# Kernel tuning notes

Measured on AMD Instinct MI355X. Metric: run time of the kernel, lower is better.

The kernel has to match this reference:

```python
import jax, jax.numpy as jnp
import numpy as np

DYNAMIC_RANGE = 16  # from init_kwargs
MAX_VAL = 2 ** (DYNAMIC_RANGE - 1) - 1   # 32767
MIN_VAL = -(2 ** (DYNAMIC_RANGE - 1))    # -32768


def setup_inputs() -> dict:
    key = jax.random.key(0)
    k_img, k_w = jax.random.split(key)
    Z, Y, X = 128, 512, 512
    P = 15                      # prediction_bands
    image = jax.random.normal(k_img, (Z, Y, X), dtype=jnp.float32) * 100.0
    # weights buffer is [num_bands, 4 + prediction_bands]; original inits to zeros
    # (degenerate output), so we use small random weights in [-1, 1].
    weights = jax.random.normal(k_w, (Z, 4 + P), dtype=jnp.float32) * 0.05
    return {"image": image, "weights": weights}


def reference(image, weights):
    # image: [Z, Y, X], weights: [Z, 4 + P]
    Z, Y, X = image.shape
    P = weights.shape[1] - 4

    # Note: sample_representatives[z] = predictions[z] + residuals[z] = image[z],
    # so all neighbor extraction operates on the raw image. Weight updates in the
    # original only touch weights[z] AFTER band z is predicted and that row is
    # never read again, so the output depends only on the initial weights.

    # Spatial neighbors (zero-padded): N, W, NW, (N+W+NW)/3  -> [Z, Y, X, 4]
    pad = jnp.pad(image, ((0, 0), (1, 1), (1, 1)))
    north = pad[:, :-2, 1:-1]
    west = pad[:, 1:-1, :-2]
    northwest = pad[:, :-2, :-2]
    fourth = (north + west + northwest) / 3
    spatial = jnp.stack([north, west, northwest, fourth], axis=-1)

    # Spectral neighbors: bands z-P .. z-1, zero-padded at the front.
    # spec_pad[z + p] == image[z - P + p] (or 0 if out of range) -> [P, Z, Y, X]
    spec_pad = jnp.concatenate(
        [jnp.zeros((P, Y, X), dtype=image.dtype), image], axis=0)
    spectral = jnp.stack([spec_pad[p:p + Z] for p in range(P)], axis=0)

    # Per-band weighted sum over the 4 + P predictors, then clamp.
    pred = (jnp.einsum('zyxs,zs->zyx', spatial, weights[:, :4])
            + jnp.einsum('pzyx,zp->zyx', spectral, weights[:, 4:]))
    pred = jnp.clip(pred, MIN_VAL, MAX_VAL)

    residuals = image - pred
    return pred, residuals
```

## Files before the change

kernel.cpp:

```cpp
#include <hip/hip_runtime.h>

#define Zdim 128
#define Ydim 512
#define Xdim 512
#define Pdim 15
#define NWt  19
#define CHUNK 32

typedef __attribute__((ext_vector_type(4))) float f4;
struct F4 { float v[4]; };

__device__ __forceinline__ F4 ld4(const float* p) {
    f4 t = *(const f4*)p;
    F4 r; r.v[0] = t[0]; r.v[1] = t[1]; r.v[2] = t[2]; r.v[3] = t[3];
    return r;
}

__global__ __launch_bounds__(256, 4) void spec_pred_kernel(
    const float* __restrict__ img,
    const float* __restrict__ wts,
    float* __restrict__ out)
{
    const int bid = blockIdx.x;
    const int zc  = bid >> 8;
    const int id  = ((bid & 255) << 8) | threadIdx.x;
    const int xg  = (id & 127) << 2;
    const int y   = id >> 7;

    const size_t plane = (size_t)Ydim * Xdim;
    const size_t pix   = (size_t)y * Xdim + xg;
    const float* ip = img + pix;
    float* pp = out + pix;
    float* rp = out + (size_t)Zdim * plane + pix;

    const int  z0 = zc * CHUNK;
    const bool hn = (y > 0);
    const bool hw = (xg > 0);

    F4 h[Pdim];
    if (z0 == 0) {
#pragma unroll
        for (int p = 0; p < Pdim; ++p) h[p] = F4{{0, 0, 0, 0}};
    } else {
#pragma unroll
        for (int p = 0; p < Pdim; ++p)
            h[p] = ld4(ip + (size_t)(z0 - Pdim + p) * plane);
    }

    F4 cb[3], nb[3];
    float wb[3], qb[3];

    auto LOAD = [&](int z, int b) {
        const float* p0 = ip + (size_t)z * plane;
        cb[b] = ld4(p0);
        nb[b] = hn ? ld4(p0 - Xdim) : F4{{0, 0, 0, 0}};
        wb[b] = hw ? p0[-1] : 0.0f;
        qb[b] = (hn && hw) ? p0[-Xdim - 1] : 0.0f;
    };

    auto STEP = [&](int z, int b) {
        const float* wz = wts + z * NWt;
        const float w3 = wz[3] * (1.0f / 3.0f);
        const float a0 = wz[0] + w3, a1 = wz[1] + w3, a2 = wz[2] + w3;
        f4 pv, rv;
#pragma unroll
        for (int e = 0; e < 4; ++e) {
            const float vn = nb[b].v[e];
            const float vw = e ? cb[b].v[e - 1] : wb[b];
            const float vq = e ? nb[b].v[e - 1] : qb[b];
            float a = a0 * vn;
            a = fmaf(a1, vw, a);
            a = fmaf(a2, vq, a);
#pragma unroll
            for (int p = 0; p < Pdim; ++p) a = fmaf(wz[4 + p], h[p].v[e], a);
            a = fminf(fmaxf(a, -32768.0f), 32767.0f);
            pv[e] = a;
            rv[e] = cb[b].v[e] - a;
        }
        __builtin_nontemporal_store(pv, (f4*)(pp + (size_t)z * plane));
        __builtin_nontemporal_store(rv, (f4*)(rp + (size_t)z * plane));
#pragma unroll
        for (int p = 0; p < Pdim - 1; ++p) h[p] = h[p + 1];
        h[Pdim - 1] = cb[b];
    };

    LOAD(z0 + 0, 0);
    LOAD(z0 + 1, 1);
#pragma unroll 6
    for (int i = 0; i < CHUNK - 2; ++i) {
        LOAD(z0 + i + 2, (i + 2) % 3);
        STEP(z0 + i, i % 3);
    }
    STEP(z0 + CHUNK - 2, (CHUNK - 2) % 3);
    STEP(z0 + CHUNK - 1, (CHUNK - 1) % 3);
}

extern "C" void kernel_launch(void* const* d_in, const int* in_sizes, int n_in,
                              void* d_out, int out_size, void* d_ws, size_t ws_size,
                              hipStream_t stream) {
    const float* img = (const float*)d_in[0];
    const float* wts = (const float*)d_in[1];
    float* out = (float*)d_out;

    const int grid = 256 * (Zdim / CHUNK);
    spec_pred_kernel<<<grid, 256, 0, stream>>>(img, wts, out);
}
```

Before: 79.42 us.

## Shuffle west neighbors, swizzle block order, use 32-bit offsets, unroll more

Lane-0 threads of each wavefront now load the west and northwest scalars from memory, and the other lanes get them from the neighboring lane with __shfl_up, which drops most scalar global loads. Blocks are remapped so that consecutive block IDs land on different row bands, and address offsets switch from size_t to unsigned to shorten address arithmetic. The FMA order is changed to start with the spectral terms, and the loop unroll goes from 6 to 15. The extra cross-lane shuffles and the larger unroll add instructions and register pressure, and the reordered FMAs can change rounding slightly.

```diff
diff --git a/kernel.cpp b/kernel.cpp
--- a/kernel.cpp
+++ b/kernel.cpp
@@ -23,19 +23,22 @@
 {
     const int bid = blockIdx.x;
     const int zc  = bid >> 8;
-    const int id  = ((bid & 255) << 8) | threadIdx.x;
+    const int r8  = bid & 255;
+    const int yb  = ((r8 & 7) << 5) | (r8 >> 3);
+    const int id  = (yb << 8) | threadIdx.x;
     const int xg  = (id & 127) << 2;
     const int y   = id >> 7;
 
-    const size_t plane = (size_t)Ydim * Xdim;
-    const size_t pix   = (size_t)y * Xdim + xg;
+    const unsigned plane = (unsigned)Ydim * Xdim;
+    const unsigned pix   = (unsigned)y * Xdim + xg;
     const float* ip = img + pix;
     float* pp = out + pix;
-    float* rp = out + (size_t)Zdim * plane + pix;
+    float* rp = out + (unsigned)Zdim * plane + pix;
 
     const int  z0 = zc * CHUNK;
     const bool hn = (y > 0);
     const bool hw = (xg > 0);
+    const bool l0 = (threadIdx.x & 63) == 0;
 
     F4 h[Pdim];
     if (z0 == 0) {
@@ -44,41 +47,43 @@
     } else {
 #pragma unroll
         for (int p = 0; p < Pdim; ++p)
-            h[p] = ld4(ip + (size_t)(z0 - Pdim + p) * plane);
+            h[p] = ld4(ip + (unsigned)(z0 - Pdim + p) * plane);
     }
 
     F4 cb[3], nb[3];
     float wb[3], qb[3];
 
     auto LOAD = [&](int z, int b) {
-        const float* p0 = ip + (size_t)z * plane;
+        const float* p0 = ip + (unsigned)z * plane;
         cb[b] = ld4(p0);
         nb[b] = hn ? ld4(p0 - Xdim) : F4{{0, 0, 0, 0}};
-        wb[b] = hw ? p0[-1] : 0.0f;
-        qb[b] = (hn && hw) ? p0[-Xdim - 1] : 0.0f;
+        wb[b] = (l0 && hw)       ? p0[-1]        : 0.0f;
+        qb[b] = (l0 && hw && hn) ? p0[-Xdim - 1] : 0.0f;
     };
 
     auto STEP = [&](int z, int b) {
         const float* wz = wts + z * NWt;
         const float w3 = wz[3] * (1.0f / 3.0f);
         const float a0 = wz[0] + w3, a1 = wz[1] + w3, a2 = wz[2] + w3;
+        float we = __shfl_up(cb[b].v[3], 1);
+        float qw = __shfl_up(nb[b].v[3], 1);
+        if (l0) { we = wb[b]; qw = qb[b]; }
         f4 pv, rv;
 #pragma unroll
         for (int e = 0; e < 4; ++e) {
             const float vn = nb[b].v[e];
-            const float vw = e ? cb[b].v[e - 1] : wb[b];
-            const float vq = e ? nb[b].v[e - 1] : qb[b];
-            float a = a0 * vn;
-            a = fmaf(a1, vw, a);
-            a = fmaf(a2, vq, a);
+            float a = wz[4] * h[0].v[e];
 #pragma unroll
-            for (int p = 0; p < Pdim; ++p) a = fmaf(wz[4 + p], h[p].v[e], a);
+            for (int p = 1; p < Pdim; ++p) a = fmaf(wz[4 + p], h[p].v[e], a);
+            a = fmaf(a0, vn, a);
+            a = fmaf(a1, e ? cb[b].v[e - 1] : we, a);
+            a = fmaf(a2, e ? nb[b].v[e - 1] : qw, a);
             a = fminf(fmaxf(a, -32768.0f), 32767.0f);
             pv[e] = a;
             rv[e] = cb[b].v[e] - a;
         }
-        __builtin_nontemporal_store(pv, (f4*)(pp + (size_t)z * plane));
-        __builtin_nontemporal_store(rv, (f4*)(rp + (size_t)z * plane));
+        __builtin_nontemporal_store(pv, (f4*)(pp + (unsigned)z * plane));
+        __builtin_nontemporal_store(rv, (f4*)(rp + (unsigned)z * plane));
 #pragma unroll
         for (int p = 0; p < Pdim - 1; ++p) h[p] = h[p + 1];
         h[Pdim - 1] = cb[b];
@@ -86,7 +91,7 @@
 
     LOAD(z0 + 0, 0);
     LOAD(z0 + 1, 1);
-#pragma unroll 6
+#pragma unroll 15
     for (int i = 0; i < CHUNK - 2; ++i) {
         LOAD(z0 + i + 2, (i + 2) % 3);
         STEP(z0 + i, i % 3);
```

New measurement: 74.47 us. 6.2% less time.
